# Kernel optimization log

Measured on AMD Instinct MI355X. Metric: run time of the kernel, lower is better.

The kernel has to match this reference:

```python
import jax, jax.numpy as jnp
import numpy as np

HID = 16
DATA_DIM = 2
B = 2048
T = 64
RTOL, ATOL = 1e-2, 1e-4
SAFETY, FMIN, FMAX = 0.9, 0.2, 10.0
MAX_STEPS = 16  # bounded adaptive-step budget (masked once t reaches T1)
T1 = 1.0
DT0 = 1.0

# Tsit5 (Tsitouras 2011) tableau
_A2 = (0.161,)
_A3 = (-0.008480655492356989, 0.335480655492357)
_A4 = (2.8971530571054935, -6.359448489975075, 4.3622954328695815)
_A5 = (5.325864828439257, -11.748883564062828, 7.4955393428898365, -0.09249506636175525)
_A6 = (5.86145544294642, -12.92096931784711, 8.159367898576159, -0.071584973281401, -0.028269050394068383)
_B5 = (0.09646076681806523, 0.01, 0.4798896504144996, 1.379008574103742, -3.290069515436081, 2.324710524099774)
_BT = (-0.00178001105222577714, -0.0008164344596567469, 0.007880878010261995, -0.1447110071732629, 0.5823571654525552, -0.45808210592918697, 0.015151515151515152)


def setup_inputs() -> dict:
    key = jax.random.key(0)
    ks = jax.random.split(key, 13)
    u = lambda k, shape, fan: jax.random.uniform(k, shape, jnp.float32, -1.0, 1.0) / np.float32(np.sqrt(fan))
    return dict(
        x_seq=jax.random.normal(ks[0], (B, T, DATA_DIM), jnp.float32),
        w1=u(ks[1], (HID, HID), HID), b1=u(ks[2], (HID,), HID),
        w2=u(ks[3], (HID, HID), HID), b2=u(ks[4], (HID,), HID),
        w3=u(ks[5], (HID, HID), HID), b3=u(ks[6], (HID,), HID),
        gru_wih=u(ks[7], (3 * HID, DATA_DIM), DATA_DIM),
        gru_whh=u(ks[8], (3 * HID, HID), HID),
        gru_b=u(ks[9], (3 * HID,), HID),
        gru_bn=u(ks[10], (HID,), HID),
        pred_w=u(ks[11], (1, HID), HID),
        pred_b=u(ks[12], (1,), HID),
    )


def _mlp(y, w1, b1, w2, b2, w3, b3):
    # eqx.nn.MLP(in=16, out=16, width=16, depth=2, activation=tanh): 3 Linear layers
    y = jnp.tanh(y @ w1.T + b1)
    y = jnp.tanh(y @ w2.T + b2)
    return y @ w3.T + b3


def _ode_solve(h0, f):
    """Adaptive Tsit5 + I-controller (diffrax PIDController defaults) from t=0 to t=1.
    Per-sample adaptive step/accept/reject, batched over the leading axis."""
    nB = h0.shape[0]

    def body(state, _):
        y, t, dt = state                      # y:[B,16]  t,dt:[B]
        dt_c = jnp.minimum(dt, T1 - t)        # clip so we never overshoot t1
        d = dt_c[:, None]
        k1 = f(y)
        k2 = f(y + d * (_A2[0] * k1))
        k3 = f(y + d * (_A3[0] * k1 + _A3[1] * k2))
        k4 = f(y + d * (_A4[0] * k1 + _A4[1] * k2 + _A4[2] * k3))
        k5 = f(y + d * (_A5[0] * k1 + _A5[1] * k2 + _A5[2] * k3 + _A5[3] * k4))
        k6 = f(y + d * (_A6[0] * k1 + _A6[1] * k2 + _A6[2] * k3 + _A6[3] * k4 + _A6[4] * k5))
        y_new = y + d * (_B5[0] * k1 + _B5[1] * k2 + _B5[2] * k3 + _B5[3] * k4 + _B5[4] * k5 + _B5[5] * k6)
        k7 = f(y_new)                          # FSAL stage, enters only the error estimate
        err = d * (_BT[0] * k1 + _BT[1] * k2 + _BT[2] * k3 + _BT[3] * k4 + _BT[4] * k5 + _BT[5] * k6 + _BT[6] * k7)
        scale = ATOL + RTOL * jnp.maximum(jnp.abs(y), jnp.abs(y_new))
        err2 = jnp.maximum(jnp.mean((err / scale) ** 2, axis=-1), 1e-16)  # squared RMS norm, [B]
        accept = err2 <= 1.0
        y = jnp.where(accept[:, None], y_new, y)
        t = jnp.where(accept, t + dt_c, t)
        # I-controller: factor = safety * err_norm**(-1/order), order=5
        factor = jnp.clip(SAFETY * err2 ** (-0.1), FMIN, FMAX)
        dt = dt_c * factor
        return (y, t, dt), None

    init = (h0, jnp.zeros((nB,), h0.dtype), jnp.full((nB,), DT0, h0.dtype))
    (y, _, _), _ = jax.lax.scan(body, init, None, length=MAX_STEPS)
    return y


def _gru(x, h, wih, whh, b, bn):
    # eqx.nn.GRUCell math
    ig = x @ wih.T + b
    hg = h @ whh.T
    ir, iz, inn = jnp.split(ig, 3, axis=-1)
    hr, hz, hn = jnp.split(hg, 3, axis=-1)
    r = jax.nn.sigmoid(ir + hr)
    z = jax.nn.sigmoid(iz + hz)
    n = jnp.tanh(inn + r * (hn + bn))
    return n + z * (h - n)


def reference(x_seq, w1, b1, w2, b2, w3, b3, gru_wih, gru_whh, gru_b, gru_bn, pred_w, pred_b):
    f = lambda y: _mlp(y, w1, b1, w2, b2, w3, b3)
    h0 = jnp.zeros((x_seq.shape[0], HID), x_seq.dtype)

    def step(h, x_t):
        h_ev = _ode_solve(h, f)
        h_new = _gru(x_t, h_ev, gru_wih, gru_whh, gru_b, gru_bn)
        return h_new, None

    xs = jnp.swapaxes(x_seq, 0, 1)  # [T, B, D]
    h_final, _ = jax.lax.scan(step, h0, xs)
    return h_final @ pred_w.T + pred_b  # [B, 1]
```

## Files before the change

kernel.cpp:

```cpp
#include <hip/hip_runtime.h>


#define T_STEPS 64
#define NB 2048
#define N_ODE_STEPS 16

typedef float v2f __attribute__((ext_vector_type(2)));
typedef int v2i __attribute__((ext_vector_type(2)));

__device__ __forceinline__ v2f make2(float a, float b) { v2f r; r.x = a; r.y = b; return r; }

#define ROR(x, r) __int_as_float(__builtin_amdgcn_update_dpp( \
    0, __float_as_int(x), 0x120 + (r), 0xF, 0xF, true))

#define ROR4_HI(x) __int_as_float(__builtin_amdgcn_update_dpp( \
    __float_as_int(x), __float_as_int(x), 0x124, 0xC, 0xF, false))

__device__ __forceinline__ float rsum16(float v) {
  v += ROR(v, 8);
  v += ROR(v, 4);
  v += ROR(v, 2);
  v += ROR(v, 1);
  return v;
}

__device__ __forceinline__ float xhalf_sum(float part) {
  v2i pr = __builtin_amdgcn_permlane32_swap(
      __float_as_int(part), __float_as_int(part), false, false);
  return __int_as_float(pr[0]) + __int_as_float(pr[1]);
}

struct G2 { v2f a, b; };

__device__ __forceinline__ G2 gather4(float x) {
  float r1 = ROR(x, 1);
  float r2 = ROR(x, 2);
  float r3 = ROR(r2, 1);
  G2 g; g.a = make2(x, r1); g.b = make2(r2, r3); return g;
}

__device__ __forceinline__ float dotG(const v2f (&WA)[2], const v2f (&WB)[2],
                                      const G2& g, float seed) {
  v2f aa = __builtin_elementwise_fma(g.a, WA[0], make2(seed, 0.0f));
  v2f bb = g.a * WB[0];
  aa = __builtin_elementwise_fma(g.b, WA[1], aa);
  bb = __builtin_elementwise_fma(g.b, WB[1], bb);
  float a  = aa.x + aa.y;
  float bs = bb.x + bb.y;
  float part = a + ROR(bs, 8);
  return ROR4_HI(xhalf_sum(part));
}

__device__ __forceinline__ float dotAB(const v2f (&WA)[2], const v2f (&WB)[2],
                                       float x, float seed) {
  G2 g = gather4(x);
  return dotG(WA, WB, g, seed);
}

__device__ __forceinline__ float tanh_res(float p) {
  return __builtin_amdgcn_rcpf(__builtin_amdgcn_exp2f(p) + 1.0f);
}

__device__ __forceinline__ float sig_p(float p) {
  float e = __builtin_amdgcn_exp2f(p);
  return __builtin_amdgcn_rcpf(1.0f + e);
}

__device__ __forceinline__ float fast_tanh(float x) {
  float e = __builtin_amdgcn_exp2f(x * 2.885390081777927f);
  return fmaf(-2.0f, __builtin_amdgcn_rcpf(e + 1.0f), 1.0f);
}

__device__ __forceinline__ float mlp_fG(const G2& g0,
    const v2f (&w1a)[2], const v2f (&w1b)[2], float b1s,
    const v2f (&w2a)[2], const v2f (&w2b)[2], float b2s,
    const v2f (&w3a)[2], const v2f (&w3b)[2], float b3s) {
  float r1v = tanh_res(dotG(w1a, w1b, g0, b1s));
  float r2v = tanh_res(dotAB(w2a, w2b, r1v, b2s));
  return dotAB(w3a, w3b, r2v, b3s);
}

__device__ __forceinline__ float mlp_f(float u,
    const v2f (&w1a)[2], const v2f (&w1b)[2], float b1s,
    const v2f (&w2a)[2], const v2f (&w2b)[2], float b2s,
    const v2f (&w3a)[2], const v2f (&w3b)[2], float b3s) {
  G2 g = gather4(u);
  return mlp_fG(g, w1a, w1b, b1s, w2a, w2b, b2s, w3a, w3b, b3s);
}

__global__
__attribute__((amdgpu_flat_work_group_size(64, 64), amdgpu_waves_per_eu(1, 1)))
void odern_kernel(
    const float* __restrict__ x_seq,
    const float* __restrict__ w1, const float* __restrict__ b1,
    const float* __restrict__ w2, const float* __restrict__ b2,
    const float* __restrict__ w3, const float* __restrict__ b3,
    const float* __restrict__ gru_wih, const float* __restrict__ gru_whh,
    const float* __restrict__ gru_b, const float* __restrict__ gru_bn,
    const float* __restrict__ pred_w, const float* __restrict__ pred_b,
    float* __restrict__ out) {
  const int tid = threadIdx.x;
  const int j = tid & 15;
  const int row16 = tid >> 4;
  const int smp = row16 & 1;
  const int hf = row16 >> 1;
  const int b = blockIdx.x * 2 + smp;
  const int jj = (j + 8) & 15;
  const int base = (j - 4 * hf) & 15;

  const float TS = 2.885390081777927f;
  const float SS = -1.4426950408889634f;
  const float N2TS = -5.770780163555854f;

  float rs2 = 0.0f, rs3 = 0.0f;
#pragma unroll
  for (int c = 0; c < 16; ++c) { rs2 += w2[j * 16 + c]; rs3 += w3[j * 16 + c]; }

  v2f w1a[2], w1b[2], w2a[2], w2b[2], w3a[2], w3b[2];
  v2f wha[2], whb[2], wza[2], wzb[2], wna[2], wnb[2];
#pragma unroll
  for (int p = 0; p < 2; ++p) {
    const int ca = (base - 2 * p) & 15;
    const int cb = (base - 2 * p - 1) & 15;
    w1a[p] = make2(w1[j * 16 + ca] * TS,  w1[j * 16 + cb] * TS);
    w1b[p] = make2(w1[jj * 16 + ca] * TS, w1[jj * 16 + cb] * TS);
    w2a[p] = make2(w2[j * 16 + ca] * N2TS,  w2[j * 16 + cb] * N2TS);
    w2b[p] = make2(w2[jj * 16 + ca] * N2TS, w2[jj * 16 + cb] * N2TS);
    w3a[p] = make2(w3[j * 16 + ca] * -2.0f,  w3[j * 16 + cb] * -2.0f);
    w3b[p] = make2(w3[jj * 16 + ca] * -2.0f, w3[jj * 16 + cb] * -2.0f);
    wha[p] = make2(gru_whh[j * 16 + ca] * SS,         gru_whh[j * 16 + cb] * SS);
    whb[p] = make2(gru_whh[jj * 16 + ca] * SS,        gru_whh[jj * 16 + cb] * SS);
    wza[p] = make2(gru_whh[(16 + j) * 16 + ca] * SS,  gru_whh[(16 + j) * 16 + cb] * SS);
    wzb[p] = make2(gru_whh[(16 + jj) * 16 + ca] * SS, gru_whh[(16 + jj) * 16 + cb] * SS);
    wna[p] = make2(gru_whh[(32 + j) * 16 + ca],  gru_whh[(32 + j) * 16 + cb]);
    wnb[p] = make2(gru_whh[(32 + jj) * 16 + ca], gru_whh[(32 + jj) * 16 + cb]);
  }
  const float b1s = hf ? 0.0f : b1[j] * TS;
  const float b2s = hf ? 0.0f : (b2[j] + rs2) * TS;
  const float b3s = hf ? 0.0f : b3[j] + rs3;
  const float wih_r0 = hf ? 0.0f : gru_wih[j * 2] * SS;
  const float wih_r1 = hf ? 0.0f : gru_wih[j * 2 + 1] * SS;
  const float wih_z0 = hf ? 0.0f : gru_wih[(16 + j) * 2] * SS;
  const float wih_z1 = hf ? 0.0f : gru_wih[(16 + j) * 2 + 1] * SS;
  const float gb_r = hf ? 0.0f : gru_b[j] * SS;
  const float gb_z = hf ? 0.0f : gru_b[16 + j] * SS;
  const float bns  = hf ? 0.0f : gru_bn[j];
  const float wih_n0 = gru_wih[(32 + base) * 2];
  const float wih_n1 = gru_wih[(32 + base) * 2 + 1];
  const float gb_n = gru_b[32 + base];
  const float pwv = pred_w[base], pbv = pred_b[0];

  const float* xp = x_seq + (size_t)b * (T_STEPS * 2);

  float hst = 0.0f;
#pragma unroll 1
  for (int t = 0; t < T_STEPS; ++t) {
    const float x0 = xp[2 * t];
    const float x1 = xp[2 * t + 1];

    float y = hst;
    float tt = 0.0f, dt = 1.0f;
    float k1 = mlp_f(y, w1a, w1b, b1s, w2a, w2b, b2s, w3a, w3b, b3s);
    float yQ1 = ROR(y, 1), yQ2 = ROR(y, 2), yQ3 = ROR(yQ2, 1);
    float kQ1 = ROR(k1, 1), kQ2 = ROR(k1, 2), kQ3 = ROR(kQ2, 1);
    v2f ya = make2(y, yQ1), yb = make2(yQ2, yQ3);
    v2f s2a = make2(0.161f * k1, 0.161f * kQ1);
    v2f s2b = make2(0.161f * kQ2, 0.161f * kQ3);
#pragma unroll 1
    for (int s = 0; s < N_ODE_STEPS; ++s) {
      if (__all(tt >= 1.0f)) break;

      const float dt_c = fminf(dt, 1.0f - tt);
      const float d = dt_c;

      v2f dd; dd.x = d; dd.y = d;
      G2 g2;
      g2.a = __builtin_elementwise_fma(dd, s2a, ya);
      g2.b = __builtin_elementwise_fma(dd, s2b, yb);
      float k2 = mlp_fG(g2, w1a, w1b, b1s, w2a, w2b, b2s, w3a, w3b, b3s);

      float s3 = fmaf(0.335480655492357f, k2, -0.008480655492356989f * k1);
      float k3 = mlp_f(fmaf(d, s3, y), w1a, w1b, b1s, w2a, w2b, b2s, w3a, w3b, b3s);

      float s4 = fmaf(4.3622954328695815f, k3,
                 fmaf(-6.359448489975075f, k2, 2.8971530571054935f * k1));
      float k4 = mlp_f(fmaf(d, s4, y), w1a, w1b, b1s, w2a, w2b, b2s, w3a, w3b, b3s);

      float s5 = fmaf(-0.09249506636175525f, k4,
                 fmaf(7.4955393428898365f, k3,
                 fmaf(-11.748883564062828f, k2, 5.325864828439257f * k1)));
      float k5 = mlp_f(fmaf(d, s5, y), w1a, w1b, b1s, w2a, w2b, b2s, w3a, w3b, b3s);

      float s6 = fmaf(-0.028269050394068383f, k5,
                 fmaf(-0.071584973281401f, k4,
                 fmaf(8.159367898576159f, k3,
                 fmaf(-12.92096931784711f, k2, 5.86145544294642f * k1))));
      float k6 = mlp_f(fmaf(d, s6, y), w1a, w1b, b1s, w2a, w2b, b2s, w3a, w3b, b3s);

      float sy = fmaf(2.324710524099774f, k6,
                 fmaf(-3.290069515436081f, k5,
                 fmaf(1.379008574103742f, k4,
                 fmaf(0.4798896504144996f, k3,
                 fmaf(0.01f, k2, 0.09646076681806523f * k1)))));
      float y_new = fmaf(d, sy, y);

      float scale4 = fmaf(0.04f, fmaxf(fabsf(y), fabsf(y_new)), 0.0004f);
      float dinv = d * __builtin_amdgcn_rcpf(scale4);

      float k7 = mlp_f(y_new, w1a, w1b, b1s, w2a, w2b, b2s, w3a, w3b, b3s);

      float se = fmaf(0.015151515151515152f, k7,
                 fmaf(-0.45808210592918697f, k6,
                 fmaf(0.5823571654525552f, k5,
                 fmaf(-0.1447110071732629f, k4,
                 fmaf(0.007880878010261995f, k3,
                 fmaf(-0.0008164344596567469f, k2, -0.001780011052225777f * k1))))));

      float r = se * dinv;
      float err2 = rsum16(r * r);

      const bool acc = err2 <= 1.0f;
      y = acc ? y_new : y;
      tt = acc ? tt + dt_c : tt;
      k1 = acc ? k7 : k1;

      float fac = __builtin_amdgcn_exp2f(
          fmaf(-0.1f, __builtin_amdgcn_logf(err2), -0.15200309344504997f));
      fac = __builtin_amdgcn_fmed3f(fac, 0.2f, 10.0f);
      dt = dt_c * fac;

      float yR1 = ROR(y, 1), yR2 = ROR(y, 2), yR3 = ROR(yR2, 1);
      float kR1 = ROR(k1, 1), kR2 = ROR(k1, 2), kR3 = ROR(kR2, 1);
      ya = make2(y, yR1); yb = make2(yR2, yR3);
      s2a = make2(0.161f * k1, 0.161f * kR1);
      s2b = make2(0.161f * kR2, 0.161f * kR3);
    }

    float ir  = fmaf(wih_r1, x1, fmaf(wih_r0, x0, gb_r));
    float iz  = fmaf(wih_z1, x1, fmaf(wih_z0, x0, gb_z));
    float in_ = fmaf(wih_n1, x1, fmaf(wih_n0, x0, gb_n));
    G2 gy = gather4(y);
    float pre_r = dotG(wha, whb, gy, ir);
    float pre_z = dotG(wza, wzb, gy, iz);
    float hnb   = dotG(wna, wnb, gy, bns);
    float rg = sig_p(pre_r);
    float zg = sig_p(pre_z);
    float ng = fast_tanh(fmaf(rg, hnb, in_));
    hst = fmaf(zg, y - ng, ng);
  }

  float ps = rsum16(hst * pwv);
  if (hf == 0 && j == 0) out[b] = ps + pbv;
}

extern "C" void kernel_launch(void* const* d_in, const int* in_sizes, int n_in,
                              void* d_out, int out_size, void* d_ws, size_t ws_size,
                              hipStream_t stream) {
  (void)in_sizes; (void)n_in; (void)out_size; (void)d_ws; (void)ws_size;
  odern_kernel<<<dim3(NB / 2), dim3(64), 0, stream>>>(
      (const float*)d_in[0],
      (const float*)d_in[1], (const float*)d_in[2],
      (const float*)d_in[3], (const float*)d_in[4],
      (const float*)d_in[5], (const float*)d_in[6],
      (const float*)d_in[7], (const float*)d_in[8],
      (const float*)d_in[9], (const float*)d_in[10],
      (const float*)d_in[11], (const float*)d_in[12],
      (float*)d_out);
}
```

Before: 169.2 us.

## Interleave two independent sample pairs per wavefront for instruction-level parallelism

Each 64-thread block now integrates four samples as two interleaved pairs (A and B) instead of two, and the grid is halved. Every MLP evaluation, error reduction and GRU update is duplicated so the two dependent chains can hide DPP and transcendental latency for each other. The earlier trick of precomputing the gathered y and k1 operands for stage 2 is dropped in favour of recomputing the gather. The cost is half as many waves across the chip, twice the per-wave instruction count, and both pairs running until the slower one finishes its adaptive steps.

```diff
diff --git a/kernel.cpp b/kernel.cpp
--- a/kernel.cpp
+++ b/kernel.cpp
@@ -51,12 +51,6 @@
   return ROR4_HI(xhalf_sum(part));
 }
 
-__device__ __forceinline__ float dotAB(const v2f (&WA)[2], const v2f (&WB)[2],
-                                       float x, float seed) {
-  G2 g = gather4(x);
-  return dotG(WA, WB, g, seed);
-}
-
 __device__ __forceinline__ float tanh_res(float p) {
   return __builtin_amdgcn_rcpf(__builtin_amdgcn_exp2f(p) + 1.0f);
 }
@@ -71,21 +65,23 @@
   return fmaf(-2.0f, __builtin_amdgcn_rcpf(e + 1.0f), 1.0f);
 }
 
-__device__ __forceinline__ float mlp_fG(const G2& g0,
+__device__ __forceinline__ void mlp2(float uA, float uB,
     const v2f (&w1a)[2], const v2f (&w1b)[2], float b1s,
     const v2f (&w2a)[2], const v2f (&w2b)[2], float b2s,
-    const v2f (&w3a)[2], const v2f (&w3b)[2], float b3s) {
-  float r1v = tanh_res(dotG(w1a, w1b, g0, b1s));
-  float r2v = tanh_res(dotAB(w2a, w2b, r1v, b2s));
-  return dotAB(w3a, w3b, r2v, b3s);
-}
-
-__device__ __forceinline__ float mlp_f(float u,
-    const v2f (&w1a)[2], const v2f (&w1b)[2], float b1s,
-    const v2f (&w2a)[2], const v2f (&w2b)[2], float b2s,
-    const v2f (&w3a)[2], const v2f (&w3b)[2], float b3s) {
-  G2 g = gather4(u);
-  return mlp_fG(g, w1a, w1b, b1s, w2a, w2b, b2s, w3a, w3b, b3s);
+    const v2f (&w3a)[2], const v2f (&w3b)[2], float b3s,
+    float& kA, float& kB) {
+  G2 gA = gather4(uA);
+  G2 gB = gather4(uB);
+  float r1A = tanh_res(dotG(w1a, w1b, gA, b1s));
+  float r1B = tanh_res(dotG(w1a, w1b, gB, b1s));
+  G2 hA = gather4(r1A);
+  G2 hB = gather4(r1B);
+  float r2A = tanh_res(dotG(w2a, w2b, hA, b2s));
+  float r2B = tanh_res(dotG(w2a, w2b, hB, b2s));
+  G2 qA = gather4(r2A);
+  G2 qB = gather4(r2B);
+  kA = dotG(w3a, w3b, qA, b3s);
+  kB = dotG(w3a, w3b, qB, b3s);
 }
 
 __global__
@@ -104,7 +100,8 @@
   const int row16 = tid >> 4;
   const int smp = row16 & 1;
   const int hf = row16 >> 1;
-  const int b = blockIdx.x * 2 + smp;
+  const int bA = blockIdx.x * 4 + smp;
+  const int bB = bA + 2;
   const int jj = (j + 8) & 15;
   const int base = (j - 4 * hf) & 15;
 
@@ -150,114 +147,153 @@
   const float gb_n = gru_b[32 + base];
   const float pwv = pred_w[base], pbv = pred_b[0];
 
-  const float* xp = x_seq + (size_t)b * (T_STEPS * 2);
-
-  float hst = 0.0f;
+  const float* xpA = x_seq + (size_t)bA * (T_STEPS * 2);
+  const float* xpB = x_seq + (size_t)bB * (T_STEPS * 2);
+
+  float hstA = 0.0f, hstB = 0.0f;
 #pragma unroll 1
   for (int t = 0; t < T_STEPS; ++t) {
-    const float x0 = xp[2 * t];
-    const float x1 = xp[2 * t + 1];
-
-    float y = hst;
-    float tt = 0.0f, dt = 1.0f;
-    float k1 = mlp_f(y, w1a, w1b, b1s, w2a, w2b, b2s, w3a, w3b, b3s);
-    float yQ1 = ROR(y, 1), yQ2 = ROR(y, 2), yQ3 = ROR(yQ2, 1);
-    float kQ1 = ROR(k1, 1), kQ2 = ROR(k1, 2), kQ3 = ROR(kQ2, 1);
-    v2f ya = make2(y, yQ1), yb = make2(yQ2, yQ3);
-    v2f s2a = make2(0.161f * k1, 0.161f * kQ1);
-    v2f s2b = make2(0.161f * kQ2, 0.161f * kQ3);
+    const float x0A = xpA[2 * t], x1A = xpA[2 * t + 1];
+    const float x0B = xpB[2 * t], x1B = xpB[2 * t + 1];
+
+    float yA = hstA, yB = hstB;
+    float ttA = 0.0f, dtA = 1.0f, ttB = 0.0f, dtB = 1.0f;
+    float k1A, k1B;
+    mlp2(yA, yB, w1a, w1b, b1s, w2a, w2b, b2s, w3a, w3b, b3s, k1A, k1B);
 #pragma unroll 1
     for (int s = 0; s < N_ODE_STEPS; ++s) {
-      if (__all(tt >= 1.0f)) break;
-
-      const float dt_c = fminf(dt, 1.0f - tt);
-      const float d = dt_c;
-
-      v2f dd; dd.x = d; dd.y = d;
-      G2 g2;
-      g2.a = __builtin_elementwise_fma(dd, s2a, ya);
-      g2.b = __builtin_elementwise_fma(dd, s2b, yb);
-      float k2 = mlp_fG(g2, w1a, w1b, b1s, w2a, w2b, b2s, w3a, w3b, b3s);
-
-      float s3 = fmaf(0.335480655492357f, k2, -0.008480655492356989f * k1);
-      float k3 = mlp_f(fmaf(d, s3, y), w1a, w1b, b1s, w2a, w2b, b2s, w3a, w3b, b3s);
-
-      float s4 = fmaf(4.3622954328695815f, k3,
-                 fmaf(-6.359448489975075f, k2, 2.8971530571054935f * k1));
-      float k4 = mlp_f(fmaf(d, s4, y), w1a, w1b, b1s, w2a, w2b, b2s, w3a, w3b, b3s);
-
-      float s5 = fmaf(-0.09249506636175525f, k4,
-                 fmaf(7.4955393428898365f, k3,
-                 fmaf(-11.748883564062828f, k2, 5.325864828439257f * k1)));
-      float k5 = mlp_f(fmaf(d, s5, y), w1a, w1b, b1s, w2a, w2b, b2s, w3a, w3b, b3s);
-
-      float s6 = fmaf(-0.028269050394068383f, k5,
-                 fmaf(-0.071584973281401f, k4,
-                 fmaf(8.159367898576159f, k3,
-                 fmaf(-12.92096931784711f, k2, 5.86145544294642f * k1))));
-      float k6 = mlp_f(fmaf(d, s6, y), w1a, w1b, b1s, w2a, w2b, b2s, w3a, w3b, b3s);
-
-      float sy = fmaf(2.324710524099774f, k6,
-                 fmaf(-3.290069515436081f, k5,
-                 fmaf(1.379008574103742f, k4,
-                 fmaf(0.4798896504144996f, k3,
-                 fmaf(0.01f, k2, 0.09646076681806523f * k1)))));
-      float y_new = fmaf(d, sy, y);
-
-      float scale4 = fmaf(0.04f, fmaxf(fabsf(y), fabsf(y_new)), 0.0004f);
-      float dinv = d * __builtin_amdgcn_rcpf(scale4);
-
-      float k7 = mlp_f(y_new, w1a, w1b, b1s, w2a, w2b, b2s, w3a, w3b, b3s);
-
-      float se = fmaf(0.015151515151515152f, k7,
-                 fmaf(-0.45808210592918697f, k6,
-                 fmaf(0.5823571654525552f, k5,
-                 fmaf(-0.1447110071732629f, k4,
-                 fmaf(0.007880878010261995f, k3,
-                 fmaf(-0.0008164344596567469f, k2, -0.001780011052225777f * k1))))));
-
-      float r = se * dinv;
-      float err2 = rsum16(r * r);
-
-      const bool acc = err2 <= 1.0f;
-      y = acc ? y_new : y;
-      tt = acc ? tt + dt_c : tt;
-      k1 = acc ? k7 : k1;
-
-      float fac = __builtin_amdgcn_exp2f(
-          fmaf(-0.1f, __builtin_amdgcn_logf(err2), -0.15200309344504997f));
-      fac = __builtin_amdgcn_fmed3f(fac, 0.2f, 10.0f);
-      dt = dt_c * fac;
-
-      float yR1 = ROR(y, 1), yR2 = ROR(y, 2), yR3 = ROR(yR2, 1);
-      float kR1 = ROR(k1, 1), kR2 = ROR(k1, 2), kR3 = ROR(kR2, 1);
-      ya = make2(y, yR1); yb = make2(yR2, yR3);
-      s2a = make2(0.161f * k1, 0.161f * kR1);
-      s2b = make2(0.161f * kR2, 0.161f * kR3);
+      if (__all((ttA >= 1.0f) && (ttB >= 1.0f))) break;
+
+      const float dA = fminf(dtA, 1.0f - ttA);
+      const float dB = fminf(dtB, 1.0f - ttB);
+
+      float k2A, k2B;
+      mlp2(fmaf(dA, 0.161f * k1A, yA), fmaf(dB, 0.161f * k1B, yB),
+           w1a, w1b, b1s, w2a, w2b, b2s, w3a, w3b, b3s, k2A, k2B);
+
+      float s3A = fmaf(0.335480655492357f, k2A, -0.008480655492356989f * k1A);
+      float s3B = fmaf(0.335480655492357f, k2B, -0.008480655492356989f * k1B);
+      float k3A, k3B;
+      mlp2(fmaf(dA, s3A, yA), fmaf(dB, s3B, yB),
+           w1a, w1b, b1s, w2a, w2b, b2s, w3a, w3b, b3s, k3A, k3B);
+
+      float s4A = fmaf(4.3622954328695815f, k3A,
+                  fmaf(-6.359448489975075f, k2A, 2.8971530571054935f * k1A));
+      float s4B = fmaf(4.3622954328695815f, k3B,
+                  fmaf(-6.359448489975075f, k2B, 2.8971530571054935f * k1B));
+      float k4A, k4B;
+      mlp2(fmaf(dA, s4A, yA), fmaf(dB, s4B, yB),
+           w1a, w1b, b1s, w2a, w2b, b2s, w3a, w3b, b3s, k4A, k4B);
+
+      float s5A = fmaf(-0.09249506636175525f, k4A,
+                  fmaf(7.4955393428898365f, k3A,
+                  fmaf(-11.748883564062828f, k2A, 5.325864828439257f * k1A)));
+      float s5B = fmaf(-0.09249506636175525f, k4B,
+                  fmaf(7.4955393428898365f, k3B,
+                  fmaf(-11.748883564062828f, k2B, 5.325864828439257f * k1B)));
+      float k5A, k5B;
+      mlp2(fmaf(dA, s5A, yA), fmaf(dB, s5B, yB),
+           w1a, w1b, b1s, w2a, w2b, b2s, w3a, w3b, b3s, k5A, k5B);
+
+      float s6A = fmaf(-0.028269050394068383f, k5A,
+                  fmaf(-0.071584973281401f, k4A,
+                  fmaf(8.159367898576159f, k3A,
+                  fmaf(-12.92096931784711f, k2A, 5.86145544294642f * k1A))));
+      float s6B = fmaf(-0.028269050394068383f, k5B,
+                  fmaf(-0.071584973281401f, k4B,
+                  fmaf(8.159367898576159f, k3B,
+                  fmaf(-12.92096931784711f, k2B, 5.86145544294642f * k1B))));
+      float k6A, k6B;
+      mlp2(fmaf(dA, s6A, yA), fmaf(dB, s6B, yB),
+           w1a, w1b, b1s, w2a, w2b, b2s, w3a, w3b, b3s, k6A, k6B);
+
+      float syA = fmaf(2.324710524099774f, k6A,
+                  fmaf(-3.290069515436081f, k5A,
+                  fmaf(1.379008574103742f, k4A,
+                  fmaf(0.4798896504144996f, k3A,
+                  fmaf(0.01f, k2A, 0.09646076681806523f * k1A)))));
+      float syB = fmaf(2.324710524099774f, k6B,
+                  fmaf(-3.290069515436081f, k5B,
+                  fmaf(1.379008574103742f, k4B,
+                  fmaf(0.4798896504144996f, k3B,
+                  fmaf(0.01f, k2B, 0.09646076681806523f * k1B)))));
+      float ynA = fmaf(dA, syA, yA);
+      float ynB = fmaf(dB, syB, yB);
+
+      float sc4A = fmaf(0.04f, fmaxf(fabsf(yA), fabsf(ynA)), 0.0004f);
+      float sc4B = fmaf(0.04f, fmaxf(fabsf(yB), fabsf(ynB)), 0.0004f);
+      float dinvA = dA * __builtin_amdgcn_rcpf(sc4A);
+      float dinvB = dB * __builtin_amdgcn_rcpf(sc4B);
+
+      float k7A, k7B;
+      mlp2(ynA, ynB, w1a, w1b, b1s, w2a, w2b, b2s, w3a, w3b, b3s, k7A, k7B);
+
+      float seA = fmaf(0.015151515151515152f, k7A,
+                  fmaf(-0.45808210592918697f, k6A,
+                  fmaf(0.5823571654525552f, k5A,
+                  fmaf(-0.1447110071732629f, k4A,
+                  fmaf(0.007880878010261995f, k3A,
+                  fmaf(-0.0008164344596567469f, k2A, -0.001780011052225777f * k1A))))));
+      float seB = fmaf(0.015151515151515152f, k7B,
+                  fmaf(-0.45808210592918697f, k6B,
+                  fmaf(0.5823571654525552f, k5B,
+                  fmaf(-0.1447110071732629f, k4B,
+                  fmaf(0.007880878010261995f, k3B,
+                  fmaf(-0.0008164344596567469f, k2B, -0.001780011052225777f * k1B))))));
+
+      float rA = seA * dinvA;
+      float rB = seB * dinvB;
+      float e2A = rsum16(rA * rA);
+      float e2B = rsum16(rB * rB);
+
+      const bool accA = e2A <= 1.0f;
+      const bool accB = e2B <= 1.0f;
+      yA = accA ? ynA : yA;  ttA = accA ? ttA + dA : ttA;  k1A = accA ? k7A : k1A;
+      yB = accB ? ynB : yB;  ttB = accB ? ttB + dB : ttB;  k1B = accB ? k7B : k1B;
+
+      float facA = __builtin_amdgcn_exp2f(
+          fmaf(-0.1f, __builtin_amdgcn_logf(e2A), -0.15200309344504997f));
+      float facB = __builtin_amdgcn_exp2f(
+          fmaf(-0.1f, __builtin_amdgcn_logf(e2B), -0.15200309344504997f));
+      dtA = dA * __builtin_amdgcn_fmed3f(facA, 0.2f, 10.0f);
+      dtB = dB * __builtin_amdgcn_fmed3f(facB, 0.2f, 10.0f);
     }
 
-    float ir  = fmaf(wih_r1, x1, fmaf(wih_r0, x0, gb_r));
-    float iz  = fmaf(wih_z1, x1, fmaf(wih_z0, x0, gb_z));
-    float in_ = fmaf(wih_n1, x1, fmaf(wih_n0, x0, gb_n));
-    G2 gy = gather4(y);
-    float pre_r = dotG(wha, whb, gy, ir);
-    float pre_z = dotG(wza, wzb, gy, iz);
-    float hnb   = dotG(wna, wnb, gy, bns);
-    float rg = sig_p(pre_r);
-    float zg = sig_p(pre_z);
-    float ng = fast_tanh(fmaf(rg, hnb, in_));
-    hst = fmaf(zg, y - ng, ng);
+    float irA = fmaf(wih_r1, x1A, fmaf(wih_r0, x0A, gb_r));
+    float izA = fmaf(wih_z1, x1A, fmaf(wih_z0, x0A, gb_z));
+    float inA = fmaf(wih_n1, x1A, fmaf(wih_n0, x0A, gb_n));
+    float irB = fmaf(wih_r1, x1B, fmaf(wih_r0, x0B, gb_r));
+    float izB = fmaf(wih_z1, x1B, fmaf(wih_z0, x0B, gb_z));
+    float inB = fmaf(wih_n1, x1B, fmaf(wih_n0, x0B, gb_n));
+    G2 gyA = gather4(yA);
+    G2 gyB = gather4(yB);
+    float prA = dotG(wha, whb, gyA, irA);
+    float prB = dotG(wha, whb, gyB, irB);
+    float pzA = dotG(wza, wzb, gyA, izA);
+    float pzB = dotG(wza, wzb, gyB, izB);
+    float hnA = dotG(wna, wnb, gyA, bns);
+    float hnB = dotG(wna, wnb, gyB, bns);
+    float rgA = sig_p(prA), rgB = sig_p(prB);
+    float zgA = sig_p(pzA), zgB = sig_p(pzB);
+    float ngA = fast_tanh(fmaf(rgA, hnA, inA));
+    float ngB = fast_tanh(fmaf(rgB, hnB, inB));
+    hstA = fmaf(zgA, yA - ngA, ngA);
+    hstB = fmaf(zgB, yB - ngB, ngB);
   }
 
-  float ps = rsum16(hst * pwv);
-  if (hf == 0 && j == 0) out[b] = ps + pbv;
+  float psA = rsum16(hstA * pwv);
+  float psB = rsum16(hstB * pwv);
+  if (hf == 0 && j == 0) {
+    out[bA] = psA + pbv;
+    out[bB] = psB + pbv;
+  }
 }
 
 extern "C" void kernel_launch(void* const* d_in, const int* in_sizes, int n_in,
                               void* d_out, int out_size, void* d_ws, size_t ws_size,
                               hipStream_t stream) {
   (void)in_sizes; (void)n_in; (void)out_size; (void)d_ws; (void)ws_size;
-  odern_kernel<<<dim3(NB / 2), dim3(64), 0, stream>>>(
+  odern_kernel<<<dim3(NB / 4), dim3(64), 0, stream>>>(
       (const float*)d_in[0],
       (const float*)d_in[1], (const float*)d_in[2],
       (const float*)d_in[3], (const float*)d_in[4],
```

Result: slower. 213.5 us (+26.2%).

## Gather eight rotated lanes per dot instead of rotating the partial sum

Applied to the files above, without the earlier changes.

The row-16 dot product now gathers eight rotated copies of the input (rotations 0-3 and 8-11) and uses column-permuted weights from the same output row. This replaces the previous scheme, which used a second output row (j+8) and rotated the partial sum by 8. The change shortens the serial dependency chain of each dot product, since the independent DPP moves can issue in parallel before the FMAs, at the cost of more DPP instructions per dot. It also drops the precomputed packed y/k1 gathers for k2 and calls the generic mlp_f path instead.

```diff
diff --git a/kernel.cpp b/kernel.cpp
--- a/kernel.cpp
+++ b/kernel.cpp
@@ -30,31 +30,26 @@
   return __int_as_float(pr[0]) + __int_as_float(pr[1]);
 }
 
-struct G2 { v2f a, b; };
-
-__device__ __forceinline__ G2 gather4(float x) {
-  float r1 = ROR(x, 1);
-  float r2 = ROR(x, 2);
-  float r3 = ROR(r2, 1);
-  G2 g; g.a = make2(x, r1); g.b = make2(r2, r3); return g;
+struct G4 { v2f a, b, c, d; };
+
+__device__ __forceinline__ G4 gatherD(float x) {
+  G4 g;
+  g.a = make2(x,          ROR(x, 1));
+  g.b = make2(ROR(x, 2),  ROR(x, 3));
+  g.c = make2(ROR(x, 8),  ROR(x, 9));
+  g.d = make2(ROR(x, 10), ROR(x, 11));
+  return g;
 }
 
 __device__ __forceinline__ float dotG(const v2f (&WA)[2], const v2f (&WB)[2],
-                                      const G2& g, float seed) {
-  v2f aa = __builtin_elementwise_fma(g.a, WA[0], make2(seed, 0.0f));
-  v2f bb = g.a * WB[0];
-  aa = __builtin_elementwise_fma(g.b, WA[1], aa);
-  bb = __builtin_elementwise_fma(g.b, WB[1], bb);
-  float a  = aa.x + aa.y;
-  float bs = bb.x + bb.y;
-  float part = a + ROR(bs, 8);
+                                      const G4& g, float seed) {
+  v2f t0 = __builtin_elementwise_fma(g.a, WA[0], make2(seed, 0.0f));
+  v2f t1 = g.b * WA[1];
+  v2f t2 = g.c * WB[0];
+  v2f t3 = g.d * WB[1];
+  v2f s = (t0 + t2) + (t1 + t3);
+  float part = s.x + s.y;
   return ROR4_HI(xhalf_sum(part));
-}
-
-__device__ __forceinline__ float dotAB(const v2f (&WA)[2], const v2f (&WB)[2],
-                                       float x, float seed) {
-  G2 g = gather4(x);
-  return dotG(WA, WB, g, seed);
 }
 
 __device__ __forceinline__ float tanh_res(float p) {
@@ -69,23 +64,18 @@
 __device__ __forceinline__ float fast_tanh(float x) {
   float e = __builtin_amdgcn_exp2f(x * 2.885390081777927f);
   return fmaf(-2.0f, __builtin_amdgcn_rcpf(e + 1.0f), 1.0f);
-}
-
-__device__ __forceinline__ float mlp_fG(const G2& g0,
-    const v2f (&w1a)[2], const v2f (&w1b)[2], float b1s,
-    const v2f (&w2a)[2], const v2f (&w2b)[2], float b2s,
-    const v2f (&w3a)[2], const v2f (&w3b)[2], float b3s) {
-  float r1v = tanh_res(dotG(w1a, w1b, g0, b1s));
-  float r2v = tanh_res(dotAB(w2a, w2b, r1v, b2s));
-  return dotAB(w3a, w3b, r2v, b3s);
 }
 
 __device__ __forceinline__ float mlp_f(float u,
     const v2f (&w1a)[2], const v2f (&w1b)[2], float b1s,
     const v2f (&w2a)[2], const v2f (&w2b)[2], float b2s,
     const v2f (&w3a)[2], const v2f (&w3b)[2], float b3s) {
-  G2 g = gather4(u);
-  return mlp_fG(g, w1a, w1b, b1s, w2a, w2b, b2s, w3a, w3b, b3s);
+  G4 g = gatherD(u);
+  float r1v = tanh_res(dotG(w1a, w1b, g, b1s));
+  G4 h = gatherD(r1v);
+  float r2v = tanh_res(dotG(w2a, w2b, h, b2s));
+  G4 q = gatherD(r2v);
+  return dotG(w3a, w3b, q, b3s);
 }
 
 __global__
@@ -105,7 +95,6 @@
   const int smp = row16 & 1;
   const int hf = row16 >> 1;
   const int b = blockIdx.x * 2 + smp;
-  const int jj = (j + 8) & 15;
   const int base = (j - 4 * hf) & 15;
 
   const float TS = 2.885390081777927f;
@@ -122,18 +111,20 @@
   for (int p = 0; p < 2; ++p) {
     const int ca = (base - 2 * p) & 15;
     const int cb = (base - 2 * p - 1) & 15;
-    w1a[p] = make2(w1[j * 16 + ca] * TS,  w1[j * 16 + cb] * TS);
-    w1b[p] = make2(w1[jj * 16 + ca] * TS, w1[jj * 16 + cb] * TS);
+    const int ca8 = ca ^ 8;
+    const int cb8 = cb ^ 8;
+    w1a[p] = make2(w1[j * 16 + ca] * TS,   w1[j * 16 + cb] * TS);
+    w1b[p] = make2(w1[j * 16 + ca8] * TS,  w1[j * 16 + cb8] * TS);
     w2a[p] = make2(w2[j * 16 + ca] * N2TS,  w2[j * 16 + cb] * N2TS);
-    w2b[p] = make2(w2[jj * 16 + ca] * N2TS, w2[jj * 16 + cb] * N2TS);
+    w2b[p] = make2(w2[j * 16 + ca8] * N2TS, w2[j * 16 + cb8] * N2TS);
     w3a[p] = make2(w3[j * 16 + ca] * -2.0f,  w3[j * 16 + cb] * -2.0f);
-    w3b[p] = make2(w3[jj * 16 + ca] * -2.0f, w3[jj * 16 + cb] * -2.0f);
-    wha[p] = make2(gru_whh[j * 16 + ca] * SS,         gru_whh[j * 16 + cb] * SS);
-    whb[p] = make2(gru_whh[jj * 16 + ca] * SS,        gru_whh[jj * 16 + cb] * SS);
+    w3b[p] = make2(w3[j * 16 + ca8] * -2.0f, w3[j * 16 + cb8] * -2.0f);
+    wha[p] = make2(gru_whh[j * 16 + ca] * SS,  gru_whh[j * 16 + cb] * SS);
+    whb[p] = make2(gru_whh[j * 16 + ca8] * SS, gru_whh[j * 16 + cb8] * SS);
     wza[p] = make2(gru_whh[(16 + j) * 16 + ca] * SS,  gru_whh[(16 + j) * 16 + cb] * SS);
-    wzb[p] = make2(gru_whh[(16 + jj) * 16 + ca] * SS, gru_whh[(16 + jj) * 16 + cb] * SS);
+    wzb[p] = make2(gru_whh[(16 + j) * 16 + ca8] * SS, gru_whh[(16 + j) * 16 + cb8] * SS);
     wna[p] = make2(gru_whh[(32 + j) * 16 + ca],  gru_whh[(32 + j) * 16 + cb]);
-    wnb[p] = make2(gru_whh[(32 + jj) * 16 + ca], gru_whh[(32 + jj) * 16 + cb]);
+    wnb[p] = make2(gru_whh[(32 + j) * 16 + ca8], gru_whh[(32 + j) * 16 + cb8]);
   }
   const float b1s = hf ? 0.0f : b1[j] * TS;
   const float b2s = hf ? 0.0f : (b2[j] + rs2) * TS;
@@ -161,11 +152,6 @@
     float y = hst;
     float tt = 0.0f, dt = 1.0f;
     float k1 = mlp_f(y, w1a, w1b, b1s, w2a, w2b, b2s, w3a, w3b, b3s);
-    float yQ1 = ROR(y, 1), yQ2 = ROR(y, 2), yQ3 = ROR(yQ2, 1);
-    float kQ1 = ROR(k1, 1), kQ2 = ROR(k1, 2), kQ3 = ROR(kQ2, 1);
-    v2f ya = make2(y, yQ1), yb = make2(yQ2, yQ3);
-    v2f s2a = make2(0.161f * k1, 0.161f * kQ1);
-    v2f s2b = make2(0.161f * kQ2, 0.161f * kQ3);
 #pragma unroll 1
     for (int s = 0; s < N_ODE_STEPS; ++s) {
       if (__all(tt >= 1.0f)) break;
@@ -173,11 +159,8 @@
       const float dt_c = fminf(dt, 1.0f - tt);
       const float d = dt_c;
 
-      v2f dd; dd.x = d; dd.y = d;
-      G2 g2;
-      g2.a = __builtin_elementwise_fma(dd, s2a, ya);
-      g2.b = __builtin_elementwise_fma(dd, s2b, yb);
-      float k2 = mlp_fG(g2, w1a, w1b, b1s, w2a, w2b, b2s, w3a, w3b, b3s);
+      float k2 = mlp_f(fmaf(d, 0.161f * k1, y),
+                       w1a, w1b, b1s, w2a, w2b, b2s, w3a, w3b, b3s);
 
       float s3 = fmaf(0.335480655492357f, k2, -0.008480655492356989f * k1);
       float k3 = mlp_f(fmaf(d, s3, y), w1a, w1b, b1s, w2a, w2b, b2s, w3a, w3b, b3s);
@@ -228,18 +211,12 @@
           fmaf(-0.1f, __builtin_amdgcn_logf(err2), -0.15200309344504997f));
       fac = __builtin_amdgcn_fmed3f(fac, 0.2f, 10.0f);
       dt = dt_c * fac;
-
-      float yR1 = ROR(y, 1), yR2 = ROR(y, 2), yR3 = ROR(yR2, 1);
-      float kR1 = ROR(k1, 1), kR2 = ROR(k1, 2), kR3 = ROR(kR2, 1);
-      ya = make2(y, yR1); yb = make2(yR2, yR3);
-      s2a = make2(0.161f * k1, 0.161f * kR1);
-      s2b = make2(0.161f * kR2, 0.161f * kR3);
     }
 
     float ir  = fmaf(wih_r1, x1, fmaf(wih_r0, x0, gb_r));
     float iz  = fmaf(wih_z1, x1, fmaf(wih_z0, x0, gb_z));
     float in_ = fmaf(wih_n1, x1, fmaf(wih_n0, x0, gb_n));
-    G2 gy = gather4(y);
+    G4 gy = gatherD(y);
     float pre_r = dotG(wha, whb, gy, ir);
     float pre_z = dotG(wza, wzb, gy, iz);
     float hnb   = dotG(wna, wnb, gy, bns);
```

Result: slower. 179.9 us (+6.4%).
